# Kernel optimization log

Hardware: AMD Instinct MI355X
Metric: run time of the kernel (lower is better)

The kernel has to match this reference:

```python
import jax, jax.numpy as jnp
import numpy as np

N_NODES = 50000
N_EDGES = 300000
F_IN, HID, N_CLS = 256, 256, 128


def _glorot_linear(key, fan_in, fan_out):
    # torch.nn.Linear-style uniform init, kaiming bound 1/sqrt(fan_in)
    s = 1.0 / np.sqrt(fan_in)
    return jax.random.uniform(key, (fan_in, fan_out), jnp.float32, -s, s)


def setup_inputs() -> dict:
    key = jax.random.key(0)
    ks = jax.random.split(key, 8)
    x = jax.random.normal(ks[0], (N_NODES, F_IN), jnp.float32)
    edge_index = jax.random.randint(ks[1], (2, N_EDGES), 0, N_NODES, dtype=jnp.int32)
    return {
        "x": x,
        "edge_index": edge_index,
        "W1": _glorot_linear(ks[2], F_IN, HID), "b1": jnp.zeros((HID,), jnp.float32),
        "W2": _glorot_linear(ks[3], HID, HID),  "b2": jnp.zeros((HID,), jnp.float32),
        "W3": _glorot_linear(ks[4], HID, HID),  "b3": jnp.zeros((HID,), jnp.float32),
        "W4": _glorot_linear(ks[5], HID, N_CLS), "b4": jnp.zeros((N_CLS,), jnp.float32),
    }


def _gcn_conv(x, W, b, src, dst, norm, n):
    # x' = D^{-1/2} (A + I) D^{-1/2} X W + b   (PyG GCNConv default)
    h = x @ W                                  # [N, out]
    msg = h[src] * norm[:, None]               # gather + edge scaling  [E', out]
    return jax.ops.segment_sum(msg, dst, num_segments=n) + b


def reference(x, edge_index, W1, b1, W2, b2, W3, b3, W4, b4):
    n = x.shape[0]
    loops = jnp.arange(n, dtype=edge_index.dtype)
    src = jnp.concatenate([edge_index[0], loops])  # add self-loops
    dst = jnp.concatenate([edge_index[1], loops])
    # symmetric normalization: deg over target nodes (unit edge weights)
    deg = jax.ops.segment_sum(jnp.ones_like(dst, jnp.float32), dst, num_segments=n)
    dis = jnp.where(deg > 0, jax.lax.rsqrt(jnp.maximum(deg, 1.0)), 0.0)
    norm = dis[src] * dis[dst]                     # [E']

    h = jax.nn.relu(_gcn_conv(x, W1, b1, src, dst, norm, n))
    h = jax.nn.relu(_gcn_conv(h, W2, b2, src, dst, norm, n))
    h = jax.nn.relu(_gcn_conv(h, W3, b3, src, dst, norm, n))
    h = _gcn_conv(h, W4, b4, src, dst, norm, n)    # [N, C]

    # global_add_pool with batch == zeros -> single-graph sum pool
    pooled = jnp.sum(h, axis=0, keepdims=True)     # [1, C]
    return (pooled, jax.nn.log_softmax(pooled, axis=1))
```

## Files before the change

kernel.cpp:

```cpp
#include <hip/hip_runtime.h>


typedef __attribute__((ext_vector_type(8))) short short8;
typedef __attribute__((ext_vector_type(8))) signed char schar8;
typedef __attribute__((ext_vector_type(4))) float float4v;

__device__ __forceinline__ unsigned short f2b(float f) {
    unsigned int u = __builtin_bit_cast(unsigned int, f);
    u += 0x7fffu + ((u >> 16) & 1u);
    return (unsigned short)(u >> 16);
}
__device__ __forceinline__ float b2f(unsigned short b) {
    unsigned int u = ((unsigned int)b) << 16;
    return __builtin_bit_cast(float, u);
}

__global__ void zero_convert_kernel(int* __restrict__ cnt, float* __restrict__ tsum,
                                    float* __restrict__ accbuf,
                                    const float* __restrict__ W1, const float* __restrict__ W2,
                                    const float* __restrict__ W3, unsigned short* __restrict__ Wt1,
                                    unsigned short* __restrict__ Wt2, unsigned short* __restrict__ Wt3,
                                    const float* __restrict__ x, unsigned short* __restrict__ xb,
                                    int N, int nb) {
    int t = threadIdx.x;
    int b = blockIdx.x;
    if (b < nb) {
        int i = b * 256 + t;
        if (i < N) { cnt[i] = 0; tsum[i] = 0.f; }
        if (b == 0) accbuf[t] = 0.f;
    } else if (b < nb + 768) {
        int bb = b - nb;
        int w = bb >> 8;
        int n = bb & 255;
        const float* W = (w == 0) ? W1 : (w == 1) ? W2 : W3;
        unsigned short* Wt = (w == 0) ? Wt1 : (w == 1) ? Wt2 : Wt3;
        Wt[n * 256 + t] = f2b(W[t * 256 + n]);
    } else {
        size_t base = ((size_t)(b - nb - 768) * 256 + t) * 8;
        if (base < (size_t)N * 256) {
            float4 lo = *(const float4*)&x[base];
            float4 hi = *(const float4*)&x[base + 4];
            uint4 o;
            o.x = (unsigned int)f2b(lo.x) | ((unsigned int)f2b(lo.y) << 16);
            o.y = (unsigned int)f2b(lo.z) | ((unsigned int)f2b(lo.w) << 16);
            o.z = (unsigned int)f2b(hi.x) | ((unsigned int)f2b(hi.y) << 16);
            o.w = (unsigned int)f2b(hi.z) | ((unsigned int)f2b(hi.w) << 16);
            *(uint4*)&xb[base] = o;
        }
    }
}

__global__ void count_kernel(const int* __restrict__ dst, int* __restrict__ cnt, int E) {
    int i = blockIdx.x * blockDim.x + threadIdx.x;
    if (i < E) atomicAdd(&cnt[dst[i]], 1);
}

__global__ void blocksum_kernel(const int* __restrict__ cnt, int* __restrict__ bsum, int N) {
    __shared__ int s[256];
    int t = threadIdx.x;
    int i = blockIdx.x * 256 + t;
    s[t] = (i < N) ? cnt[i] : 0;
    __syncthreads();
    for (int d = 128; d > 0; d >>= 1) {
        if (t < d) s[t] += s[t + d];
        __syncthreads();
    }
    if (t == 0) bsum[blockIdx.x] = s[0];
}

__global__ void finalize_kernel(const int* __restrict__ cnt, const int* __restrict__ bsum,
                                int* __restrict__ offs, int* __restrict__ cursor,
                                float* __restrict__ dis, int N, int E, int nb) {
    __shared__ int bs[256];
    __shared__ int s[256];
    int t = threadIdx.x;
    bs[t] = (t < nb) ? bsum[t] : 0;
    __syncthreads();
    for (int d = 1; d < 256; d <<= 1) {
        int x = (t >= d) ? bs[t - d] : 0;
        __syncthreads();
        bs[t] += x;
        __syncthreads();
    }
    int blockoff = (blockIdx.x == 0) ? 0 : bs[blockIdx.x - 1];
    int i = blockIdx.x * 256 + t;
    int c = (i < N) ? cnt[i] : 0;
    s[t] = c;
    __syncthreads();
    for (int d = 1; d < 256; d <<= 1) {
        int x = (t >= d) ? s[t - d] : 0;
        __syncthreads();
        s[t] += x;
        __syncthreads();
    }
    if (i < N) {
        int ex = blockoff + s[t] - c;
        offs[i] = ex;
        cursor[i] = ex;
        dis[i] = rsqrtf((float)(c + 1));
    }
    if (blockIdx.x == 0 && t == 0) offs[N] = E;
}

__global__ void scatter_outsum_kernel(const int* __restrict__ src, const int* __restrict__ dst,
                                      const float* __restrict__ dis, int* __restrict__ cursor,
                                      int* __restrict__ csr_src, float* __restrict__ csr_nrm,
                                      float* __restrict__ tsum, int E) {
    int i = blockIdx.x * blockDim.x + threadIdx.x;
    if (i < E) {
        int s = src[i], d = dst[i];
        float dd = dis[d];
        int pos = atomicAdd(&cursor[d], 1);
        csr_src[pos] = s;
        csr_nrm[pos] = dis[s] * dd;
        atomicAdd(&tsum[s], dd);
    }
}

__global__ __launch_bounds__(256, 2) void gemm_bf16_kernel(
        const unsigned short* __restrict__ Ab, const unsigned short* __restrict__ Wt,
        signed char* __restrict__ C8, float* __restrict__ Ts, int M) {
    __shared__ unsigned short As[2 * 128 * 64];
    __shared__ unsigned short Bs[2 * 128 * 64];
    const int tid = threadIdx.x;
    const int lane = tid & 63;
    const int wave = tid >> 6;
    const int l15 = lane & 15;
    const int quad = lane >> 4;
    const int wm = wave & 1;
    const int wn = wave >> 1;

    const int bid = blockIdx.x;
    const int grp = bid >> 4;
    const int ii = bid & 15;
    const int xv = grp * 8 + (ii & 7);
    const int yv = ii >> 3;
    const int m0 = xv * 128;
    const int n0 = yv * 128;
    if (m0 >= M) return;

    float4v acc[4][4] = {};

    const int lrow = lane >> 3;
    const int lslot = (lane & 7) ^ lrow;

    const unsigned short* Bt = Wt + (size_t)n0 * 256;

#define GSTAGE(bufofs, kk)                                                          \
    {                                                                               \
        _Pragma("unroll") for (int i_ = 0; i_ < 4; i_++) {                          \
            int r0 = wave * 32 + i_ * 8;                                            \
            int gm = m0 + r0 + lrow;                                                \
            if (gm >= M) gm = M - 1;                                                \
            const unsigned short* gp = &Ab[(size_t)gm * 256 + (kk) + lslot * 8];    \
            __builtin_amdgcn_global_load_lds(                                       \
                (const __attribute__((address_space(1))) unsigned int*)gp,          \
                (__attribute__((address_space(3))) unsigned int*)&As[(bufofs) + r0 * 64], \
                16, 0, 0);                                                          \
        }                                                                           \
        _Pragma("unroll") for (int i_ = 0; i_ < 4; i_++) {                          \
            int r0 = wave * 32 + i_ * 8;                                            \
            const unsigned short* gp = &Bt[(size_t)(r0 + lrow) * 256 + (kk) + lslot * 8]; \
            __builtin_amdgcn_global_load_lds(                                       \
                (const __attribute__((address_space(1))) unsigned int*)gp,          \
                (__attribute__((address_space(3))) unsigned int*)&Bs[(bufofs) + r0 * 64], \
                16, 0, 0);                                                          \
        }                                                                           \
    }

    GSTAGE(0, 0);
    __syncthreads();
    int cur = 0;
#pragma unroll
    for (int s = 0; s < 4; ++s) {
        if (s < 3) GSTAGE((cur ^ 1) * 8192, (s + 1) * 64);
        __builtin_amdgcn_sched_barrier(0);
        const unsigned short* Ac = &As[cur * 8192];
        const unsigned short* Bc = &Bs[cur * 8192];
#pragma unroll
        for (int ks = 0; ks < 64; ks += 32) {
            const int sl = (ks >> 3) + quad;
            short8 af[4], bf[4];
#pragma unroll
            for (int mi = 0; mi < 4; mi++) {
                int row = wm * 64 + mi * 16 + l15;
                af[mi] = *(const short8*)&Ac[row * 64 + 8 * (sl ^ (row & 7))];
            }
#pragma unroll
            for (int nj = 0; nj < 4; nj++) {
                int row = wn * 64 + nj * 16 + l15;
                bf[nj] = *(const short8*)&Bc[row * 64 + 8 * (sl ^ (row & 7))];
            }
#pragma unroll
            for (int mi = 0; mi < 4; mi++)
#pragma unroll
                for (int nj = 0; nj < 4; nj++)
                    acc[mi][nj] = __builtin_amdgcn_mfma_f32_16x16x32_bf16(
                        af[mi], bf[nj], acc[mi][nj], 0, 0, 0);
        }
        __syncthreads();
        cur ^= 1;
    }
#undef GSTAGE

    float* pmax = (float*)As;
    float* pinv = (float*)Bs;
#pragma unroll
    for (int mi = 0; mi < 4; mi++) {
#pragma unroll
        for (int r = 0; r < 4; r++) {
            float m = fabsf(acc[mi][0][r]);
            m = fmaxf(m, fabsf(acc[mi][1][r]));
            m = fmaxf(m, fabsf(acc[mi][2][r]));
            m = fmaxf(m, fabsf(acc[mi][3][r]));
            m = fmaxf(m, __shfl_xor(m, 1));
            m = fmaxf(m, __shfl_xor(m, 2));
            m = fmaxf(m, __shfl_xor(m, 4));
            m = fmaxf(m, __shfl_xor(m, 8));
            if (l15 == 0) pmax[(wm * 64 + mi * 16 + quad * 4 + r) * 2 + wn] = m;
        }
    }
    __syncthreads();
    if (tid < 128) {
        float m = fmaxf(pmax[tid * 2], pmax[tid * 2 + 1]);
        int grow = m0 + tid;
        if (grow < M) Ts[(size_t)grow * 2 + yv] = m * (1.f / 127.f);
        pinv[tid] = (m > 0.f) ? 127.f / m : 0.f;
    }
    __syncthreads();
#pragma unroll
    for (int mi = 0; mi < 4; mi++) {
#pragma unroll
        for (int r = 0; r < 4; r++) {
            int lr = wm * 64 + mi * 16 + quad * 4 + r;
            float inv = pinv[lr];
            int row = m0 + lr;
            if (row < M) {
#pragma unroll
                for (int nj = 0; nj < 4; nj++) {
                    int col = n0 + wn * 64 + nj * 16 + l15;
                    C8[(size_t)row * 256 + col] =
                        (signed char)__float2int_rn(acc[mi][nj][r] * inv);
                }
            }
        }
    }
}

template <int RELU>
__global__ __launch_bounds__(256) void agg_bf16_kernel(
        const signed char* __restrict__ T8, const float* __restrict__ Ts,
        const float* __restrict__ bias,
        const int* __restrict__ offs, const int* __restrict__ csr_src,
        const float* __restrict__ csr_nrm, const float* __restrict__ dis,
        unsigned short* __restrict__ out, int N) {
    int hw = threadIdx.x >> 5;
    int l = threadIdx.x & 31;
    int v = blockIdx.x * 8 + hw;
    if (v >= N) return;
    int f8 = l * 8;
    int hh = l >> 4;
    int beg = offs[v], end = offs[v + 1];
    float dv = dis[v];
    float w = dv * dv * Ts[(size_t)v * 2 + hh];
    float a[8];
    {
        schar8 q = *(const schar8*)&T8[(size_t)v * 256 + f8];
#pragma unroll
        for (int i = 0; i < 8; i++) a[i] = w * (float)q[i];
    }
    int e = beg;
    for (; e + 4 <= end; e += 4) {
        int s0 = csr_src[e],     s1 = csr_src[e + 1];
        int s2 = csr_src[e + 2], s3 = csr_src[e + 3];
        float n0 = csr_nrm[e]     * Ts[(size_t)s0 * 2 + hh];
        float n1 = csr_nrm[e + 1] * Ts[(size_t)s1 * 2 + hh];
        float n2 = csr_nrm[e + 2] * Ts[(size_t)s2 * 2 + hh];
        float n3 = csr_nrm[e + 3] * Ts[(size_t)s3 * 2 + hh];
        schar8 h0 = *(const schar8*)&T8[(size_t)s0 * 256 + f8];
        schar8 h1 = *(const schar8*)&T8[(size_t)s1 * 256 + f8];
        schar8 h2 = *(const schar8*)&T8[(size_t)s2 * 256 + f8];
        schar8 h3 = *(const schar8*)&T8[(size_t)s3 * 256 + f8];
#pragma unroll
        for (int i = 0; i < 8; i++)
            a[i] += n0 * (float)h0[i] + n1 * (float)h1[i]
                  + n2 * (float)h2[i] + n3 * (float)h3[i];
    }
    for (; e < end; e++) {
        int s = csr_src[e];
        float nm = csr_nrm[e] * Ts[(size_t)s * 2 + hh];
        schar8 h = *(const schar8*)&T8[(size_t)s * 256 + f8];
#pragma unroll
        for (int i = 0; i < 8; i++) a[i] += nm * (float)h[i];
    }
    float4 bv0 = *(const float4*)&bias[f8];
    float4 bv1 = *(const float4*)&bias[f8 + 4];
    a[0] += bv0.x; a[1] += bv0.y; a[2] += bv0.z; a[3] += bv0.w;
    a[4] += bv1.x; a[5] += bv1.y; a[6] += bv1.z; a[7] += bv1.w;
    if (RELU) {
#pragma unroll
        for (int i = 0; i < 8; i++) a[i] = fmaxf(a[i], 0.f);
    }
    uint4 o;
    o.x = (unsigned int)f2b(a[0]) | ((unsigned int)f2b(a[1]) << 16);
    o.y = (unsigned int)f2b(a[2]) | ((unsigned int)f2b(a[3]) << 16);
    o.z = (unsigned int)f2b(a[4]) | ((unsigned int)f2b(a[5]) << 16);
    o.w = (unsigned int)f2b(a[6]) | ((unsigned int)f2b(a[7]) << 16);
    *(uint4*)&out[(size_t)v * 256 + f8] = o;
}

__global__ __launch_bounds__(256) void wpool_partial(
        const unsigned short* __restrict__ H, const float* __restrict__ dis,
        const float* __restrict__ tsum, float* __restrict__ partial, int N) {
    int tid = threadIdx.x;
    int f8 = (tid & 31) * 8;
    int rg = tid >> 5;
    float a[8] = {};
    for (int r = blockIdx.x * 8 + rg; r < N; r += gridDim.x * 8) {
        float s = dis[r] * (dis[r] + tsum[r]);
        short8 h = *(const short8*)&H[(size_t)r * 256 + f8];
#pragma unroll
        for (int i = 0; i < 8; i++) a[i] += s * b2f((unsigned short)h[i]);
    }
    __shared__ float red[8 * 256];
#pragma unroll
    for (int i = 0; i < 8; i++) red[rg * 256 + f8 + i] = a[i];
    __syncthreads();
    for (int s = 4; s > 0; s >>= 1) {
        if (rg < s) {
#pragma unroll
            for (int i = 0; i < 8; i++)
                red[rg * 256 + f8 + i] += red[(rg + s) * 256 + f8 + i];
        }
        __syncthreads();
    }
    partial[(size_t)blockIdx.x * 256 + tid] = red[tid];
}

__global__ void wpool_reduce(const float* __restrict__ partial, float* __restrict__ acc) {
    int f = threadIdx.x;
    int p0 = blockIdx.x * 32;
    float a = 0.f;
#pragma unroll
    for (int p = 0; p < 32; p++) a += partial[(size_t)(p0 + p) * 256 + f];
    atomicAdd(&acc[f], a);
}

__global__ void final_kernel(const float* __restrict__ acc, const float* __restrict__ W4,
                             const float* __restrict__ b4, float* __restrict__ out, int N) {
    __shared__ float red[128];
    int c = threadIdx.x;
    float p = (float)N * b4[c];
    for (int k = 0; k < 256; k++) p += acc[k] * W4[k * 128 + c];
    out[c] = p;
    red[c] = p;
    __syncthreads();
    for (int s = 64; s > 0; s >>= 1) {
        if (c < s) red[c] = fmaxf(red[c], red[c + s]);
        __syncthreads();
    }
    float m = red[0];
    __syncthreads();
    red[c] = expf(p - m);
    __syncthreads();
    for (int s = 64; s > 0; s >>= 1) {
        if (c < s) red[c] += red[c + s];
        __syncthreads();
    }
    float lse = m + logf(red[0]);
    out[128 + c] = p - lse;
}

extern "C" void kernel_launch(void* const* d_in, const int* in_sizes, int n_in,
                              void* d_out, int out_size, void* d_ws, size_t ws_size,
                              hipStream_t stream) {
    const float* x  = (const float*)d_in[0];
    const int*   ei = (const int*)d_in[1];
    const float* W1 = (const float*)d_in[2];
    const float* b1 = (const float*)d_in[3];
    const float* W2 = (const float*)d_in[4];
    const float* b2 = (const float*)d_in[5];
    const float* W3 = (const float*)d_in[6];
    const float* b3 = (const float*)d_in[7];
    const float* W4 = (const float*)d_in[8];
    const float* b4 = (const float*)d_in[9];

    const int N = in_sizes[0] / 256;
    const int E = in_sizes[1] / 2;
    const int* src = ei;
    const int* dst = ei + E;

    char* p = (char*)d_ws;
    auto alloc = [&](size_t bytes) {
        char* r = p;
        p += (bytes + 255) & ~(size_t)255;
        return r;
    };
    int*            cnt     = (int*)alloc((size_t)N * 4);
    int*            offs    = (int*)alloc((size_t)(N + 1) * 4);
    int*            cursor  = (int*)alloc((size_t)N * 4);
    float*          dis     = (float*)alloc((size_t)N * 4);
    float*          tsum    = (float*)alloc((size_t)N * 4);
    int*            bsum    = (int*)alloc(1024 * 4);
    int*            csr_src = (int*)alloc((size_t)E * 4);
    float*          csr_nrm = (float*)alloc((size_t)E * 4);
    unsigned short* Wt1     = (unsigned short*)alloc(256 * 256 * 2);
    unsigned short* Wt2     = (unsigned short*)alloc(256 * 256 * 2);
    unsigned short* Wt3     = (unsigned short*)alloc(256 * 256 * 2);
    unsigned short* xb      = (unsigned short*)alloc((size_t)N * 256 * 2);
    signed char*    T8      = (signed char*)alloc((size_t)N * 256);
    float*          Ts      = (float*)alloc((size_t)N * 2 * 4);
    unsigned short* Abuf    = (unsigned short*)alloc((size_t)N * 256 * 2);
    float*          partial = (float*)alloc((size_t)1024 * 256 * 4);
    float*          accbuf  = (float*)alloc(256 * 4);

    int eb = (E + 255) / 256;
    int nb = (N + 255) / 256;
    int ncvt = (N * 32 + 255) / 256;
    zero_convert_kernel<<<nb + 768 + ncvt, 256, 0, stream>>>(
        cnt, tsum, accbuf, W1, W2, W3, Wt1, Wt2, Wt3, x, xb, N, nb);
    count_kernel<<<eb, 256, 0, stream>>>(dst, cnt, E);
    blocksum_kernel<<<nb, 256, 0, stream>>>(cnt, bsum, N);
    finalize_kernel<<<nb, 256, 0, stream>>>(cnt, bsum, offs, cursor, dis, N, E, nb);
    scatter_outsum_kernel<<<eb, 256, 0, stream>>>(src, dst, dis, cursor, csr_src,
                                                  csr_nrm, tsum, E);

    int mtiles = (N + 127) / 128;
    int ggrid = ((mtiles + 7) / 8) * 16;
    int ab = (N + 7) / 8;
    gemm_bf16_kernel<<<ggrid, 256, 0, stream>>>(xb, Wt1, T8, Ts, N);
    agg_bf16_kernel<1><<<ab, 256, 0, stream>>>(T8, Ts, b1, offs, csr_src, csr_nrm, dis, Abuf, N);
    gemm_bf16_kernel<<<ggrid, 256, 0, stream>>>(Abuf, Wt2, T8, Ts, N);
    agg_bf16_kernel<1><<<ab, 256, 0, stream>>>(T8, Ts, b2, offs, csr_src, csr_nrm, dis, Abuf, N);
    gemm_bf16_kernel<<<ggrid, 256, 0, stream>>>(Abuf, Wt3, T8, Ts, N);
    agg_bf16_kernel<1><<<ab, 256, 0, stream>>>(T8, Ts, b3, offs, csr_src, csr_nrm, dis, Abuf, N);

    wpool_partial<<<1024, 256, 0, stream>>>(Abuf, dis, tsum, partial, N);
    wpool_reduce<<<32, 256, 0, stream>>>(partial, accbuf);
    final_kernel<<<1, 128, 0, stream>>>(accbuf, W4, b4, (float*)d_out, N);
}
```

Before: 306.6 us.

## Load full A tile into LDS once and read B fragments directly from global

The GEMM now stages the entire 128x256 A tile into LDS in a single pass with an XOR swizzle, instead of a double-buffered K pipeline. The B (weight) fragments are read straight from global memory, relying on the small weight matrix staying cached in L2/L1, which removes the LDS staging for B and the per-stage barriers. The trade-off is that A loading no longer overlaps with compute, and the direct global B reads may add latency on each MFMA step. The LDS footprint stays the same at 64KB, so occupancy is unchanged.

```diff
diff --git a/kernel.cpp b/kernel.cpp
--- a/kernel.cpp
+++ b/kernel.cpp
@@ -120,8 +120,7 @@
 __global__ __launch_bounds__(256, 2) void gemm_bf16_kernel(
         const unsigned short* __restrict__ Ab, const unsigned short* __restrict__ Wt,
         signed char* __restrict__ C8, float* __restrict__ Ts, int M) {
-    __shared__ unsigned short As[2 * 128 * 64];
-    __shared__ unsigned short Bs[2 * 128 * 64];
+    __shared__ unsigned short As[128 * 256];
     const int tid = threadIdx.x;
     const int lane = tid & 63;
     const int wave = tid >> 6;
@@ -141,70 +140,48 @@
 
     float4v acc[4][4] = {};
 
-    const int lrow = lane >> 3;
-    const int lslot = (lane & 7) ^ lrow;
+    const int rl = lane >> 5;
+    const int sc = lane & 31;
+#pragma unroll
+    for (int i = 0; i < 16; i++) {
+        int r0 = wave * 32 + i * 2;
+        int row = r0 + rl;
+        int gm = m0 + row;
+        if (gm >= M) gm = M - 1;
+        const unsigned short* gp = &Ab[(size_t)gm * 256 + 8 * (sc ^ (row & 7))];
+        __builtin_amdgcn_global_load_lds(
+            (const __attribute__((address_space(1))) unsigned int*)gp,
+            (__attribute__((address_space(3))) unsigned int*)&As[r0 * 256],
+            16, 0, 0);
+    }
+    __syncthreads();
 
     const unsigned short* Bt = Wt + (size_t)n0 * 256;
-
-#define GSTAGE(bufofs, kk)                                                          \
-    {                                                                               \
-        _Pragma("unroll") for (int i_ = 0; i_ < 4; i_++) {                          \
-            int r0 = wave * 32 + i_ * 8;                                            \
-            int gm = m0 + r0 + lrow;                                                \
-            if (gm >= M) gm = M - 1;                                                \
-            const unsigned short* gp = &Ab[(size_t)gm * 256 + (kk) + lslot * 8];    \
-            __builtin_amdgcn_global_load_lds(                                       \
-                (const __attribute__((address_space(1))) unsigned int*)gp,          \
-                (__attribute__((address_space(3))) unsigned int*)&As[(bufofs) + r0 * 64], \
-                16, 0, 0);                                                          \
-        }                                                                           \
-        _Pragma("unroll") for (int i_ = 0; i_ < 4; i_++) {                          \
-            int r0 = wave * 32 + i_ * 8;                                            \
-            const unsigned short* gp = &Bt[(size_t)(r0 + lrow) * 256 + (kk) + lslot * 8]; \
-            __builtin_amdgcn_global_load_lds(                                       \
-                (const __attribute__((address_space(1))) unsigned int*)gp,          \
-                (__attribute__((address_space(3))) unsigned int*)&Bs[(bufofs) + r0 * 64], \
-                16, 0, 0);                                                          \
-        }                                                                           \
-    }
-
-    GSTAGE(0, 0);
-    __syncthreads();
-    int cur = 0;
-#pragma unroll
-    for (int s = 0; s < 4; ++s) {
-        if (s < 3) GSTAGE((cur ^ 1) * 8192, (s + 1) * 64);
-        __builtin_amdgcn_sched_barrier(0);
-        const unsigned short* Ac = &As[cur * 8192];
-        const unsigned short* Bc = &Bs[cur * 8192];
-#pragma unroll
-        for (int ks = 0; ks < 64; ks += 32) {
-            const int sl = (ks >> 3) + quad;
-            short8 af[4], bf[4];
-#pragma unroll
-            for (int mi = 0; mi < 4; mi++) {
-                int row = wm * 64 + mi * 16 + l15;
-                af[mi] = *(const short8*)&Ac[row * 64 + 8 * (sl ^ (row & 7))];
-            }
-#pragma unroll
-            for (int nj = 0; nj < 4; nj++) {
-                int row = wn * 64 + nj * 16 + l15;
-                bf[nj] = *(const short8*)&Bc[row * 64 + 8 * (sl ^ (row & 7))];
-            }
-#pragma unroll
-            for (int mi = 0; mi < 4; mi++)
-#pragma unroll
-                for (int nj = 0; nj < 4; nj++)
-                    acc[mi][nj] = __builtin_amdgcn_mfma_f32_16x16x32_bf16(
-                        af[mi], bf[nj], acc[mi][nj], 0, 0, 0);
-        }
-        __syncthreads();
-        cur ^= 1;
-    }
-#undef GSTAGE
+#pragma unroll
+    for (int kc = 0; kc < 256; kc += 32) {
+        const int sl = (kc >> 3) + quad;
+        short8 af[4], bf[4];
+#pragma unroll
+        for (int mi = 0; mi < 4; mi++) {
+            int row = wm * 64 + mi * 16 + l15;
+            af[mi] = *(const short8*)&As[row * 256 + 8 * (sl ^ (row & 7))];
+        }
+#pragma unroll
+        for (int nj = 0; nj < 4; nj++) {
+            int row = wn * 64 + nj * 16 + l15;
+            bf[nj] = *(const short8*)&Bt[(size_t)row * 256 + kc + quad * 8];
+        }
+#pragma unroll
+        for (int mi = 0; mi < 4; mi++)
+#pragma unroll
+            for (int nj = 0; nj < 4; nj++)
+                acc[mi][nj] = __builtin_amdgcn_mfma_f32_16x16x32_bf16(
+                    af[mi], bf[nj], acc[mi][nj], 0, 0, 0);
+    }
+    __syncthreads();
 
     float* pmax = (float*)As;
-    float* pinv = (float*)Bs;
+    float* pinv = (float*)&As[2048];
 #pragma unroll
     for (int mi = 0; mi < 4; mi++) {
 #pragma unroll
```

Result: slower. 335.1 us (+9.3%).
